# Kernel tuning notes

Measured on AMD Instinct MI355X. Metric: run time of the kernel, lower is better.

The kernel has to match this reference:

```python
import jax, jax.numpy as jnp
import numpy as np

N_USERS, N_MOVIES, M, K = 100000, 20000, 8, 32
B = 524288

def setup_inputs() -> dict:
    key = jax.random.key(0)
    k1, k2, k3, k4 = jax.random.split(key, 4)
    edge = jax.random.randint(k1, (B, 2), 0, 20000, dtype=jnp.int64) if jax.config.jax_enable_x64 else jax.random.randint(k1, (B, 2), 0, 20000, dtype=jnp.int32)
    std = 1.0 / K
    taste_emb = jax.random.normal(k2, (N_USERS, M * K), dtype=jnp.float32) * std
    attn_emb = jax.random.normal(k3, (N_USERS, M * K), dtype=jnp.float32) * std
    movie_emb = jax.random.normal(k4, (N_MOVIES, K), dtype=jnp.float32) * std
    user_bias = jnp.zeros((N_USERS, 1), dtype=jnp.float32)
    movie_bias = jnp.zeros((N_MOVIES, 1), dtype=jnp.float32)
    return {"edge": edge, "taste_emb": taste_emb, "attn_emb": attn_emb,
            "movie_emb": movie_emb, "user_bias": user_bias, "movie_bias": movie_bias}

def reference(edge, taste_emb, attn_emb, movie_emb, user_bias, movie_bias):
    u = edge[:, 0]
    v = edge[:, 1]
    A = attn_emb[u].reshape(-1, M, K)   # [B, m, k]
    U = taste_emb[u].reshape(-1, M, K)  # [B, m, k]
    e = movie_emb[v]                    # [B, k]
    logits = jnp.einsum('bmk,bk->bm', A, e)          # bmm(A, e) -> [B, m]
    att = jax.nn.softmax(logits, axis=1)             # softmax over m tastes
    scores = jnp.einsum('bmk,bk->bm', U, e)          # bmm(U, e) -> [B, m]
    y_hat = jnp.sum(scores * att, axis=1) + movie_bias[v, 0] + user_bias[u, 0]
    return y_hat  # [B]
```

## Files before the change

### kernel.cpp

```cpp
#include <hip/hip_runtime.h>


#define MOT_CAP     64
#define MOT_OVF_CAP 4096

__device__ __forceinline__ float mot_score(const float* __restrict__ Ar,
                                           const float* __restrict__ Tr,
                                           const float4* __restrict__ Ep) {
    float4 ek[8];
    #pragma unroll
    for (int k4 = 0; k4 < 8; ++k4) ek[k4] = Ep[k4];
    float num = 0.f, den = 0.f;
    #pragma unroll
    for (int m = 0; m < 8; ++m) {
        float l = 0.f, s = 0.f;
        #pragma unroll
        for (int k4 = 0; k4 < 8; ++k4) {
            const float4 a = *(const float4*)(Ar + m * 32 + k4 * 4);
            const float4 t = *(const float4*)(Tr + m * 32 + k4 * 4);
            const float4 e = ek[k4];
            l = fmaf(a.x, e.x, l); l = fmaf(a.y, e.y, l);
            l = fmaf(a.z, e.z, l); l = fmaf(a.w, e.w, l);
            s = fmaf(t.x, e.x, s); s = fmaf(t.y, e.y, s);
            s = fmaf(t.z, e.z, s); s = fmaf(t.w, e.w, s);
        }
        const float ex = __expf(l);
        den += ex;
        num = fmaf(ex, s, num);
    }
    return num / den;
}

__global__ void mot_scatter_kernel(const int4* __restrict__ edge2,
                                   int* __restrict__ cnt,
                                   int* __restrict__ ovfMeta,
                                   int* __restrict__ ovf,
                                   int2* __restrict__ sve,
                                   int nPairs, int nEdges) {
    const int i = blockIdx.x * 256 + (int)threadIdx.x;
    if (i < nPairs) {
        const int4 q = edge2[i];
        int pos = atomicAdd(&cnt[q.x], 1);
        if (pos < MOT_CAP) sve[(size_t)q.x * MOT_CAP + pos] = make_int2(q.y, 2 * i);
        else { int o = atomicAdd(ovfMeta, 1); if (o < MOT_OVF_CAP) ovf[o] = 2 * i; }
        pos = atomicAdd(&cnt[q.z], 1);
        if (pos < MOT_CAP) sve[(size_t)q.z * MOT_CAP + pos] = make_int2(q.w, 2 * i + 1);
        else { int o = atomicAdd(ovfMeta, 1); if (o < MOT_OVF_CAP) ovf[o] = 2 * i + 1; }
    } else if (i == nPairs && (nEdges & 1)) {
        const int2 e = ((const int2*)edge2)[nEdges - 1];
        int pos = atomicAdd(&cnt[e.x], 1);
        if (pos < MOT_CAP) sve[(size_t)e.x * MOT_CAP + pos] = make_int2(e.y, nEdges - 1);
        else { int o = atomicAdd(ovfMeta, 1); if (o < MOT_OVF_CAP) ovf[o] = nEdges - 1; }
    }
}

__global__ __launch_bounds__(256, 4) void mot_main_kernel(
    const int2* __restrict__ edge,
    const float* __restrict__ taste_emb,
    const float* __restrict__ attn_emb,
    const float4* __restrict__ movie_emb,
    const float* __restrict__ user_bias,
    const float* __restrict__ movie_bias,
    const int* __restrict__ cnt,
    const int2* __restrict__ sve,
    const int* __restrict__ ovfMeta,
    const int* __restrict__ ovf,
    float* __restrict__ out,
    int nUsers)
{
    const int lane = (int)threadIdx.x & 63;
    const int wid  = blockIdx.x * 4 + ((int)threadIdx.x >> 6);

    if (wid < nUsers) {
        const int u = __builtin_amdgcn_readfirstlane(wid);
        int n = cnt[u];
        n = n > MOT_CAP ? MOT_CAP : n;
        if (n == 0) return;
        int2 ve = make_int2(0, -1);
        if (lane < n) ve = sve[(size_t)u * MOT_CAP + lane];
        const float y = mot_score(attn_emb  + (size_t)u * 256,
                                  taste_emb + (size_t)u * 256,
                                  movie_emb + (size_t)ve.x * 8)
                        + user_bias[u] + movie_bias[ve.x];
        if (ve.y >= 0) out[ve.y] = y;
    } else {
        int oc = ovfMeta[0];
        if (oc > MOT_OVF_CAP) oc = MOT_OVF_CAP;
        const int oi = (wid - nUsers) * 64 + lane;
        if (oi < oc) {
            const int eid = ovf[oi];
            const int2 ed = edge[eid];
            out[eid] = mot_score(attn_emb  + (size_t)ed.x * 256,
                                 taste_emb + (size_t)ed.x * 256,
                                 movie_emb + (size_t)ed.y * 8)
                       + user_bias[ed.x] + movie_bias[ed.y];
        }
    }
}

__global__ __launch_bounds__(256, 4) void mot_flat_kernel(
    const int2* __restrict__ edge,
    const float4* __restrict__ taste_emb,
    const float4* __restrict__ attn_emb,
    const float4* __restrict__ movie_emb,
    const float* __restrict__ user_bias,
    const float* __restrict__ movie_bias,
    float* __restrict__ out,
    int nEdges)
{
    const int tid  = blockIdx.x * 256 + (int)threadIdx.x;
    const int eid  = tid >> 5;
    const int s    = tid & 31;
    if (eid >= nEdges) return;
    const int2 ed = edge[eid];
    const int u = ed.x, v = ed.y;
    const float4* Ap = attn_emb  + (size_t)u * 64;
    const float4* Tp = taste_emb + (size_t)u * 64;
    const float4* Ep = movie_emb + (size_t)v * 8;
    const float4 a0 = Ap[2 * s], a1 = Ap[2 * s + 1];
    const float4 t0 = Tp[2 * s], t1 = Tp[2 * s + 1];
    const int c = s & 3;
    const float4 e0 = Ep[2 * c], e1 = Ep[2 * c + 1];
    float lp = a0.x*e0.x + a0.y*e0.y + a0.z*e0.z + a0.w*e0.w
             + a1.x*e1.x + a1.y*e1.y + a1.z*e1.z + a1.w*e1.w;
    float sp = t0.x*e0.x + t0.y*e0.y + t0.z*e0.z + t0.w*e0.w
             + t1.x*e1.x + t1.y*e1.y + t1.z*e1.z + t1.w*e1.w;
    lp += __shfl_xor(lp, 1); lp += __shfl_xor(lp, 2);
    sp += __shfl_xor(sp, 1); sp += __shfl_xor(sp, 2);
    const float ex = __expf(lp);
    float den = ex, num = ex * sp;
    den += __shfl_xor(den, 4);  num += __shfl_xor(num, 4);
    den += __shfl_xor(den, 8);  num += __shfl_xor(num, 8);
    den += __shfl_xor(den, 16); num += __shfl_xor(num, 16);
    if (s == 0) out[eid] = num / den + user_bias[u] + movie_bias[v];
}

extern "C" void kernel_launch(void* const* d_in, const int* in_sizes, int n_in,
                              void* d_out, int out_size, void* d_ws, size_t ws_size,
                              hipStream_t stream) {
    const int2*   edge       = (const int2*)d_in[0];
    const float*  taste_emb  = (const float*)d_in[1];
    const float*  attn_emb   = (const float*)d_in[2];
    const float*  movie_emb  = (const float*)d_in[3];
    const float*  user_bias  = (const float*)d_in[4];
    const float*  movie_bias = (const float*)d_in[5];
    float*        out        = (float*)d_out;

    const int nEdges = in_sizes[0] / 2;
    const int NB     = in_sizes[3] / 32;

    auto align256 = [](size_t x) { return (x + 255) & ~(size_t)255; };
    char* ws = (char*)d_ws;

    const size_t o_cnt  = 0;
    const size_t o_meta = align256((size_t)NB * 4);
    const size_t o_ovf  = o_meta + 256;
    const size_t o_sve  = align256(o_ovf + (size_t)MOT_OVF_CAP * 4);
    const size_t need   = o_sve + (size_t)NB * MOT_CAP * 8;

    if (ws_size < need) {
        const int blocks = (nEdges * 32 + 255) / 256;
        mot_flat_kernel<<<blocks, 256, 0, stream>>>(
            edge, (const float4*)taste_emb, (const float4*)attn_emb,
            (const float4*)movie_emb, user_bias, movie_bias, out, nEdges);
        return;
    }

    int*  cnt     = (int*)(ws + o_cnt);
    int*  ovfMeta = (int*)(ws + o_meta);
    int*  ovf     = (int*)(ws + o_ovf);
    int2* sve     = (int2*)(ws + o_sve);

    hipMemsetAsync(ws, 0, o_ovf, stream);

    const int nPairs  = nEdges / 2;
    const int sblocks = (nPairs + 1 + 255) / 256;
    mot_scatter_kernel<<<sblocks, 256, 0, stream>>>(
        (const int4*)edge, cnt, ovfMeta, ovf, sve, nPairs, nEdges);

    const int ublocks = (NB + 3) / 4 + (MOT_OVF_CAP / 64 + 3) / 4;
    mot_main_kernel<<<ublocks, 256, 0, stream>>>(
        edge, taste_emb, attn_emb, (const float4*)movie_emb,
        user_bias, movie_bias, cnt, sve, ovfMeta, ovf, out, NB);
}
```

Measured before the change: 72.17 us.

## Stage user embedding rows in LDS and process half-wave per user

Each block now loads the attn and taste rows of 8 users cooperatively into shared memory, and each half-wave (32 lanes) handles one user's bucket, looping over edges in chunks of 32. The per-edge inner loop reads the user rows from LDS instead of through wave-uniform global loads, and the division is replaced by a hardware reciprocal. The change targets the scalar/global load overhead of reading 2 KB per user per lane group, and gives better lane use for users with at most 32 edges. In exchange it adds a barrier, 16 KB of LDS per block, and possible LDS bank conflicts from broadcast float4 reads.

```diff
diff --git a/kernel.cpp b/kernel.cpp
--- a/kernel.cpp
+++ b/kernel.cpp
@@ -4,9 +4,9 @@
 #define MOT_CAP     64
 #define MOT_OVF_CAP 4096
 
-__device__ __forceinline__ float mot_score(const float* __restrict__ Ar,
-                                           const float* __restrict__ Tr,
-                                           const float4* __restrict__ Ep) {
+__device__ __forceinline__ float mot_score_div(const float* __restrict__ Ar,
+                                               const float* __restrict__ Tr,
+                                               const float4* __restrict__ Ep) {
     float4 ek[8];
     #pragma unroll
     for (int k4 = 0; k4 < 8; ++k4) ek[k4] = Ep[k4];
@@ -66,33 +66,79 @@
     const int* __restrict__ ovfMeta,
     const int* __restrict__ ovf,
     float* __restrict__ out,
-    int nUsers)
+    int nUsers, int mainBlocks)
 {
-    const int lane = (int)threadIdx.x & 63;
-    const int wid  = blockIdx.x * 4 + ((int)threadIdx.x >> 6);
-
-    if (wid < nUsers) {
-        const int u = __builtin_amdgcn_readfirstlane(wid);
+    __shared__ float4 sA[8 * 64];
+    __shared__ float4 sT[8 * 64];
+
+    const int tid = (int)threadIdx.x;
+
+    if ((int)blockIdx.x < mainBlocks) {
+        const int u0 = (int)blockIdx.x * 8;
+        const int nu = (nUsers - u0) < 8 ? (nUsers - u0) : 8;
+        {
+            const float4* __restrict__ srcA = (const float4*)(attn_emb)  + (size_t)u0 * 64;
+            const float4* __restrict__ srcT = (const float4*)(taste_emb) + (size_t)u0 * 64;
+            const int nf = nu * 64;
+            for (int i = tid; i < nf; i += 256) { sA[i] = srcA[i]; sT[i] = srcT[i]; }
+        }
+        __syncthreads();
+
+        const int lane = tid & 63;
+        const int us   = (tid >> 6) * 2 + (lane >> 5);
+        const int s    = lane & 31;
+        const int u    = u0 + us;
+        if (us >= nu) return;
+
         int n = cnt[u];
         n = n > MOT_CAP ? MOT_CAP : n;
         if (n == 0) return;
-        int2 ve = make_int2(0, -1);
-        if (lane < n) ve = sve[(size_t)u * MOT_CAP + lane];
-        const float y = mot_score(attn_emb  + (size_t)u * 256,
-                                  taste_emb + (size_t)u * 256,
-                                  movie_emb + (size_t)ve.x * 8)
-                        + user_bias[u] + movie_bias[ve.x];
-        if (ve.y >= 0) out[ve.y] = y;
+
+        const float  ub = user_bias[u];
+        const float4* __restrict__ Arow = sA + us * 64;
+        const float4* __restrict__ Trow = sT + us * 64;
+        const int2*  __restrict__ bucket = sve + (size_t)u * MOT_CAP;
+
+        for (int base = 0; base < n; base += 32) {
+            const int ei = base + s;
+            if (ei < n) {
+                const int2 ve = bucket[ei];
+                const float4* __restrict__ Ep = movie_emb + (size_t)ve.x * 8;
+                float4 ek[8];
+                #pragma unroll
+                for (int k4 = 0; k4 < 8; ++k4) ek[k4] = Ep[k4];
+
+                float num = 0.f, den = 0.f;
+                #pragma unroll
+                for (int m = 0; m < 8; ++m) {
+                    float l = 0.f, sc = 0.f;
+                    #pragma unroll
+                    for (int k4 = 0; k4 < 8; ++k4) {
+                        const float4 a = Arow[m * 8 + k4];
+                        const float4 t = Trow[m * 8 + k4];
+                        const float4 e = ek[k4];
+                        l  = fmaf(a.x, e.x, l);  l  = fmaf(a.y, e.y, l);
+                        l  = fmaf(a.z, e.z, l);  l  = fmaf(a.w, e.w, l);
+                        sc = fmaf(t.x, e.x, sc); sc = fmaf(t.y, e.y, sc);
+                        sc = fmaf(t.z, e.z, sc); sc = fmaf(t.w, e.w, sc);
+                    }
+                    const float ex = __expf(l);
+                    den += ex;
+                    num = fmaf(ex, sc, num);
+                }
+                out[ve.y] = num * __builtin_amdgcn_rcpf(den) + ub + movie_bias[ve.x];
+            }
+        }
     } else {
         int oc = ovfMeta[0];
         if (oc > MOT_OVF_CAP) oc = MOT_OVF_CAP;
-        const int oi = (wid - nUsers) * 64 + lane;
+        const int oi = ((int)blockIdx.x - mainBlocks) * 256 + tid;
         if (oi < oc) {
             const int eid = ovf[oi];
             const int2 ed = edge[eid];
-            out[eid] = mot_score(attn_emb  + (size_t)ed.x * 256,
-                                 taste_emb + (size_t)ed.x * 256,
-                                 movie_emb + (size_t)ed.y * 8)
+            out[eid] = mot_score_div(attn_emb  + (size_t)ed.x * 256,
+                                     taste_emb + (size_t)ed.x * 256,
+                                     movie_emb + (size_t)ed.y * 8)
                        + user_bias[ed.x] + movie_bias[ed.y];
         }
     }
@@ -178,8 +224,9 @@
     mot_scatter_kernel<<<sblocks, 256, 0, stream>>>(
         (const int4*)edge, cnt, ovfMeta, ovf, sve, nPairs, nEdges);
 
-    const int ublocks = (NB + 3) / 4 + (MOT_OVF_CAP / 64 + 3) / 4;
-    mot_main_kernel<<<ublocks, 256, 0, stream>>>(
+    const int mainBlocks = (NB + 7) / 8;
+    const int ovfBlocks  = MOT_OVF_CAP / 256;
+    mot_main_kernel<<<mainBlocks + ovfBlocks, 256, 0, stream>>>(
         edge, taste_emb, attn_emb, (const float4*)movie_emb,
-        user_bias, movie_bias, cnt, sve, ovfMeta, ovf, out, NB);
-}
+        user_bias, movie_bias, cnt, sve, ovfMeta, ovf, out, NB, mainBlocks);
+}
```

Measured after the change: 72.68 us. Within noise of the previous version (+0.7%).

## Replace capped per-user buckets with counting sort of edges by user

Applied to the files above, without the earlier changes.

Swaps the fixed-capacity per-user bucket scatter plus overflow list for an exact counting sort. The new pipeline is histogram, single-block scan, then scatter into a dense sorted array. A flat per-edge kernel then processes edges in user order, so neighbouring threads share user rows in cache. This removes the idle lanes that came from one wavefront per user with few edges, and drops the overflow path. In exchange it adds two extra kernel launches and a serial single-block scan over 20000 entries.

```diff
diff --git a/kernel.cpp b/kernel.cpp
--- a/kernel.cpp
+++ b/kernel.cpp
@@ -1,101 +1,109 @@
 #include <hip/hip_runtime.h>
 
 
-#define MOT_CAP     64
-#define MOT_OVF_CAP 4096
+__global__ void mot_zero_kernel(int4* __restrict__ p, int n4) {
+    const int i = blockIdx.x * 256 + (int)threadIdx.x;
+    if (i < n4) p[i] = make_int4(0, 0, 0, 0);
+}
 
-__device__ __forceinline__ float mot_score(const float* __restrict__ Ar,
-                                           const float* __restrict__ Tr,
-                                           const float4* __restrict__ Ep) {
+__global__ void mot_hist_kernel(const int4* __restrict__ edge2, int* __restrict__ hist,
+                                int nPairs, int nEdges) {
+    const int i = blockIdx.x * 256 + (int)threadIdx.x;
+    if (i < nPairs) {
+        const int4 q = edge2[i];
+        atomicAdd(&hist[q.x], 1);
+        atomicAdd(&hist[q.z], 1);
+    } else if (i == nPairs && (nEdges & 1)) {
+        atomicAdd(&hist[((const int2*)edge2)[nEdges - 1].x], 1);
+    }
+}
+
+__global__ __launch_bounds__(1024) void mot_scan_kernel(const int* __restrict__ hist,
+                                                        int* __restrict__ cursor, int n) {
+    const int T = 1024;
+    const int t = (int)threadIdx.x;
+    const int chunk = (n + T - 1) / T;
+    const int lo = t * chunk;
+    const int hi = (lo + chunk) < n ? (lo + chunk) : n;
+    int sum = 0;
+    for (int i = lo; i < hi; ++i) sum += hist[i];
+
+    const int lane = t & 63, w = t >> 6;
+    int incl = sum;
+    for (int off = 1; off < 64; off <<= 1) {
+        int x = __shfl_up(incl, off);
+        if (lane >= off) incl += x;
+    }
+    __shared__ int wsum[16];
+    if (lane == 63) wsum[w] = incl;
+    __syncthreads();
+    int woff = 0;
+    for (int k = 0; k < w; ++k) woff += wsum[k];
+    int run = woff + incl - sum;
+    for (int i = lo; i < hi; ++i) {
+        cursor[i] = run;
+        run += hist[i];
+    }
+}
+
+__global__ void mot_scatter_kernel(const int4* __restrict__ edge2, int* __restrict__ cursor,
+                                   int4* __restrict__ sve4, int nPairs, int nEdges) {
+    const int i = blockIdx.x * 256 + (int)threadIdx.x;
+    if (i < nPairs) {
+        const int4 q = edge2[i];
+        int pos = atomicAdd(&cursor[q.x], 1);
+        sve4[pos] = make_int4(q.x, q.y, 2 * i, 0);
+        pos = atomicAdd(&cursor[q.z], 1);
+        sve4[pos] = make_int4(q.z, q.w, 2 * i + 1, 0);
+    } else if (i == nPairs && (nEdges & 1)) {
+        const int2 e = ((const int2*)edge2)[nEdges - 1];
+        int pos = atomicAdd(&cursor[e.x], 1);
+        sve4[pos] = make_int4(e.x, e.y, nEdges - 1, 0);
+    }
+}
+
+__global__ __launch_bounds__(256, 4) void mot_edge_kernel(
+    const int4* __restrict__ sve4,
+    const float4* __restrict__ taste_emb,
+    const float4* __restrict__ attn_emb,
+    const float4* __restrict__ movie_emb,
+    const float* __restrict__ user_bias,
+    const float* __restrict__ movie_bias,
+    float* __restrict__ out,
+    int nEdges)
+{
+    const int i = blockIdx.x * 256 + (int)threadIdx.x;
+    if (i >= nEdges) return;
+    const int4 e = sve4[i];
+
+    const float4* __restrict__ Ap = attn_emb  + (size_t)e.x * 64;
+    const float4* __restrict__ Tp = taste_emb + (size_t)e.x * 64;
+    const float4* __restrict__ Ep = movie_emb + (size_t)e.y * 8;
+
     float4 ek[8];
     #pragma unroll
     for (int k4 = 0; k4 < 8; ++k4) ek[k4] = Ep[k4];
+
     float num = 0.f, den = 0.f;
     #pragma unroll
     for (int m = 0; m < 8; ++m) {
+        float4 av[8], tv[8];
+        #pragma unroll
+        for (int k4 = 0; k4 < 8; ++k4) { av[k4] = Ap[m * 8 + k4]; tv[k4] = Tp[m * 8 + k4]; }
         float l = 0.f, s = 0.f;
         #pragma unroll
         for (int k4 = 0; k4 < 8; ++k4) {
-            const float4 a = *(const float4*)(Ar + m * 32 + k4 * 4);
-            const float4 t = *(const float4*)(Tr + m * 32 + k4 * 4);
-            const float4 e = ek[k4];
-            l = fmaf(a.x, e.x, l); l = fmaf(a.y, e.y, l);
-            l = fmaf(a.z, e.z, l); l = fmaf(a.w, e.w, l);
-            s = fmaf(t.x, e.x, s); s = fmaf(t.y, e.y, s);
-            s = fmaf(t.z, e.z, s); s = fmaf(t.w, e.w, s);
+            const float4 a = av[k4], t = tv[k4], v = ek[k4];
+            l = fmaf(a.x, v.x, l); l = fmaf(a.y, v.y, l);
+            l = fmaf(a.z, v.z, l); l = fmaf(a.w, v.w, l);
+            s = fmaf(t.x, v.x, s); s = fmaf(t.y, v.y, s);
+            s = fmaf(t.z, v.z, s); s = fmaf(t.w, v.w, s);
         }
         const float ex = __expf(l);
         den += ex;
         num = fmaf(ex, s, num);
     }
-    return num / den;
-}
-
-__global__ void mot_scatter_kernel(const int4* __restrict__ edge2,
-                                   int* __restrict__ cnt,
-                                   int* __restrict__ ovfMeta,
-                                   int* __restrict__ ovf,
-                                   int2* __restrict__ sve,
-                                   int nPairs, int nEdges) {
-    const int i = blockIdx.x * 256 + (int)threadIdx.x;
-    if (i < nPairs) {
-        const int4 q = edge2[i];
-        int pos = atomicAdd(&cnt[q.x], 1);
-        if (pos < MOT_CAP) sve[(size_t)q.x * MOT_CAP + pos] = make_int2(q.y, 2 * i);
-        else { int o = atomicAdd(ovfMeta, 1); if (o < MOT_OVF_CAP) ovf[o] = 2 * i; }
-        pos = atomicAdd(&cnt[q.z], 1);
-        if (pos < MOT_CAP) sve[(size_t)q.z * MOT_CAP + pos] = make_int2(q.w, 2 * i + 1);
-        else { int o = atomicAdd(ovfMeta, 1); if (o < MOT_OVF_CAP) ovf[o] = 2 * i + 1; }
-    } else if (i == nPairs && (nEdges & 1)) {
-        const int2 e = ((const int2*)edge2)[nEdges - 1];
-        int pos = atomicAdd(&cnt[e.x], 1);
-        if (pos < MOT_CAP) sve[(size_t)e.x * MOT_CAP + pos] = make_int2(e.y, nEdges - 1);
-        else { int o = atomicAdd(ovfMeta, 1); if (o < MOT_OVF_CAP) ovf[o] = nEdges - 1; }
-    }
-}
-
-__global__ __launch_bounds__(256, 4) void mot_main_kernel(
-    const int2* __restrict__ edge,
-    const float* __restrict__ taste_emb,
-    const float* __restrict__ attn_emb,
-    const float4* __restrict__ movie_emb,
-    const float* __restrict__ user_bias,
-    const float* __restrict__ movie_bias,
-    const int* __restrict__ cnt,
-    const int2* __restrict__ sve,
-    const int* __restrict__ ovfMeta,
-    const int* __restrict__ ovf,
-    float* __restrict__ out,
-    int nUsers)
-{
-    const int lane = (int)threadIdx.x & 63;
-    const int wid  = blockIdx.x * 4 + ((int)threadIdx.x >> 6);
-
-    if (wid < nUsers) {
-        const int u = __builtin_amdgcn_readfirstlane(wid);
-        int n = cnt[u];
-        n = n > MOT_CAP ? MOT_CAP : n;
-        if (n == 0) return;
-        int2 ve = make_int2(0, -1);
-        if (lane < n) ve = sve[(size_t)u * MOT_CAP + lane];
-        const float y = mot_score(attn_emb  + (size_t)u * 256,
-                                  taste_emb + (size_t)u * 256,
-                                  movie_emb + (size_t)ve.x * 8)
-                        + user_bias[u] + movie_bias[ve.x];
-        if (ve.y >= 0) out[ve.y] = y;
-    } else {
-        int oc = ovfMeta[0];
-        if (oc > MOT_OVF_CAP) oc = MOT_OVF_CAP;
-        const int oi = (wid - nUsers) * 64 + lane;
-        if (oi < oc) {
-            const int eid = ovf[oi];
-            const int2 ed = edge[eid];
-            out[eid] = mot_score(attn_emb  + (size_t)ed.x * 256,
-                                 taste_emb + (size_t)ed.x * 256,
-                                 movie_emb + (size_t)ed.y * 8)
-                       + user_bias[ed.x] + movie_bias[ed.y];
-        }
-    }
+    out[e.z] = num * __builtin_amdgcn_rcpf(den) + user_bias[e.x] + movie_bias[e.y];
 }
 
 __global__ __launch_bounds__(256, 4) void mot_flat_kernel(
@@ -152,11 +160,10 @@
     auto align256 = [](size_t x) { return (x + 255) & ~(size_t)255; };
     char* ws = (char*)d_ws;
 
-    const size_t o_cnt  = 0;
-    const size_t o_meta = align256((size_t)NB * 4);
-    const size_t o_ovf  = o_meta + 256;
-    const size_t o_sve  = align256(o_ovf + (size_t)MOT_OVF_CAP * 4);
-    const size_t need   = o_sve + (size_t)NB * MOT_CAP * 8;
+    const size_t o_hist = 0;
+    const size_t o_cur  = align256((size_t)NB * 4);
+    const size_t o_sve  = align256(o_cur + (size_t)NB * 4);
+    const size_t need   = o_sve + (size_t)nEdges * 16;
 
     if (ws_size < need) {
         const int blocks = (nEdges * 32 + 255) / 256;
@@ -166,20 +173,22 @@
         return;
     }
 
-    int*  cnt     = (int*)(ws + o_cnt);
-    int*  ovfMeta = (int*)(ws + o_meta);
-    int*  ovf     = (int*)(ws + o_ovf);
-    int2* sve     = (int2*)(ws + o_sve);
+    int*  hist   = (int*)(ws + o_hist);
+    int*  cursor = (int*)(ws + o_cur);
+    int4* sve4   = (int4*)(ws + o_sve);
 
-    hipMemsetAsync(ws, 0, o_ovf, stream);
+    const int n4 = (int)(align256((size_t)NB * 4) / 16);
+    mot_zero_kernel<<<(n4 + 255) / 256, 256, 0, stream>>>((int4*)hist, n4);
 
     const int nPairs  = nEdges / 2;
     const int sblocks = (nPairs + 1 + 255) / 256;
-    mot_scatter_kernel<<<sblocks, 256, 0, stream>>>(
-        (const int4*)edge, cnt, ovfMeta, ovf, sve, nPairs, nEdges);
+    mot_hist_kernel<<<sblocks, 256, 0, stream>>>((const int4*)edge, hist, nPairs, nEdges);
+    mot_scan_kernel<<<1, 1024, 0, stream>>>(hist, cursor, NB);
+    mot_scatter_kernel<<<sblocks, 256, 0, stream>>>((const int4*)edge, cursor, sve4,
+                                                    nPairs, nEdges);
 
-    const int ublocks = (NB + 3) / 4 + (MOT_OVF_CAP / 64 + 3) / 4;
-    mot_main_kernel<<<ublocks, 256, 0, stream>>>(
-        edge, taste_emb, attn_emb, (const float4*)movie_emb,
-        user_bias, movie_bias, cnt, sve, ovfMeta, ovf, out, NB);
+    const int eblocks = (nEdges + 255) / 256;
+    mot_edge_kernel<<<eblocks, 256, 0, stream>>>(
+        sve4, (const float4*)taste_emb, (const float4*)attn_emb,
+        (const float4*)movie_emb, user_bias, movie_bias, out, nEdges);
 }
```

New measurement: 141.3 us. 95.7% more time.

## Compute per-user logits with fp16 MFMA and replace memset with zero kernel

Applied to the files above, without the earlier changes.

The per-user main kernel now loads each user's 16 attention and taste rows once into an fp16 MFMA A-operand. It processes up to 16 movies per 16x16x32 MFMA, then redistributes the results with lane shuffles for the softmax. This replaces the per-lane scalar FMA loops, where every lane re-read the full 2 KB of user rows. It also swaps hipMemsetAsync for a custom zero kernel and uses a reciprocal instead of division. The fp16 conversion of embeddings and the approximate reciprocal reduce numerical precision.

```diff
diff --git a/kernel.cpp b/kernel.cpp
--- a/kernel.cpp
+++ b/kernel.cpp
@@ -4,9 +4,17 @@
 #define MOT_CAP     64
 #define MOT_OVF_CAP 4096
 
-__device__ __forceinline__ float mot_score(const float* __restrict__ Ar,
-                                           const float* __restrict__ Tr,
-                                           const float4* __restrict__ Ep) {
+using half8 = __attribute__((ext_vector_type(8))) _Float16;
+using f32x4 = __attribute__((ext_vector_type(4))) float;
+
+__global__ void mot_zero_kernel(int4* __restrict__ p, int n4) {
+    const int i = blockIdx.x * 256 + (int)threadIdx.x;
+    if (i < n4) p[i] = make_int4(0, 0, 0, 0);
+}
+
+__device__ __forceinline__ float mot_score_div(const float* __restrict__ Ar,
+                                               const float* __restrict__ Tr,
+                                               const float4* __restrict__ Ep) {
     float4 ek[8];
     #pragma unroll
     for (int k4 = 0; k4 < 8; ++k4) ek[k4] = Ep[k4];
@@ -54,7 +62,7 @@
     }
 }
 
-__global__ __launch_bounds__(256, 4) void mot_main_kernel(
+__global__ __launch_bounds__(256, 4) void mot_mfma_kernel(
     const int2* __restrict__ edge,
     const float* __restrict__ taste_emb,
     const float* __restrict__ attn_emb,
@@ -66,33 +74,92 @@
     const int* __restrict__ ovfMeta,
     const int* __restrict__ ovf,
     float* __restrict__ out,
-    int nUsers)
+    int nUsers, int mainBlocks)
 {
-    const int lane = (int)threadIdx.x & 63;
-    const int wid  = blockIdx.x * 4 + ((int)threadIdx.x >> 6);
-
-    if (wid < nUsers) {
-        const int u = __builtin_amdgcn_readfirstlane(wid);
+    const int tid  = (int)threadIdx.x;
+    const int lane = tid & 63;
+
+    if ((int)blockIdx.x < mainBlocks) {
+        const int u = (int)blockIdx.x * 4 + (tid >> 6);
+        if (u >= nUsers) return;
         int n = cnt[u];
         n = n > MOT_CAP ? MOT_CAP : n;
         if (n == 0) return;
-        int2 ve = make_int2(0, -1);
-        if (lane < n) ve = sve[(size_t)u * MOT_CAP + lane];
-        const float y = mot_score(attn_emb  + (size_t)u * 256,
-                                  taste_emb + (size_t)u * 256,
-                                  movie_emb + (size_t)ve.x * 8)
-                        + user_bias[u] + movie_bias[ve.x];
-        if (ve.y >= 0) out[ve.y] = y;
+
+        const int row = lane & 15;
+        const int kq  = lane >> 4;
+        const int k0  = kq * 8;
+
+        const float* rowp = (row < 8)
+            ? attn_emb  + (size_t)u * 256 + row * 32 + k0
+            : taste_emb + (size_t)u * 256 + (row - 8) * 32 + k0;
+        const float4 r0 = *(const float4*)rowp;
+        const float4 r1 = *(const float4*)(rowp + 4);
+        half8 af;
+        af[0] = (_Float16)r0.x; af[1] = (_Float16)r0.y;
+        af[2] = (_Float16)r0.z; af[3] = (_Float16)r0.w;
+        af[4] = (_Float16)r1.x; af[5] = (_Float16)r1.y;
+        af[6] = (_Float16)r1.z; af[7] = (_Float16)r1.w;
+
+        const float ub = user_bias[u];
+        const int2* __restrict__ bucket = sve + (size_t)u * MOT_CAP;
+        const int hi = kq & 1;
+
+        for (int t = 0; t < n; t += 16) {
+            const int ei = t + row;
+            const bool valid = ei < n;
+            const int2 ve = valid ? bucket[ei] : make_int2(0, -1);
+
+            half8 bf = {};
+            if (valid) {
+                const float4* __restrict__ Ep = movie_emb + (size_t)ve.x * 8;
+                const float4 e0 = Ep[kq * 2];
+                const float4 e1 = Ep[kq * 2 + 1];
+                bf[0] = (_Float16)e0.x; bf[1] = (_Float16)e0.y;
+                bf[2] = (_Float16)e0.z; bf[3] = (_Float16)e0.w;
+                bf[4] = (_Float16)e1.x; bf[5] = (_Float16)e1.y;
+                bf[6] = (_Float16)e1.z; bf[7] = (_Float16)e1.w;
+            }
+
+            f32x4 c = {0.f, 0.f, 0.f, 0.f};
+            c = __builtin_amdgcn_mfma_f32_16x16x32_f16(af, bf, c, 0, 0, 0);
+
+            const float o0 = __shfl_xor(c[0], 16);
+            const float o1 = __shfl_xor(c[1], 16);
+            const float o2 = __shfl_xor(c[2], 16);
+            const float o3 = __shfl_xor(c[3], 16);
+            float v0 = hi ? o0 : c[0], v1 = hi ? o1 : c[1];
+            float v2 = hi ? o2 : c[2], v3 = hi ? o3 : c[3];
+            float v4 = hi ? c[0] : o0, v5 = hi ? c[1] : o1;
+            float v6 = hi ? c[2] : o2, v7 = hi ? c[3] : o3;
+            const float w0 = __shfl_xor(v0, 32), w1 = __shfl_xor(v1, 32);
+            const float w2 = __shfl_xor(v2, 32), w3 = __shfl_xor(v3, 32);
+            const float w4 = __shfl_xor(v4, 32), w5 = __shfl_xor(v5, 32);
+            const float w6 = __shfl_xor(v6, 32), w7 = __shfl_xor(v7, 32);
+
+            if (kq == 0 && valid) {
+                float den = 0.f, num = 0.f;
+                const float e0x = __expf(v0); den += e0x; num = fmaf(e0x, w0, num);
+                const float e1x = __expf(v1); den += e1x; num = fmaf(e1x, w1, num);
+                const float e2x = __expf(v2); den += e2x; num = fmaf(e2x, w2, num);
+                const float e3x = __expf(v3); den += e3x; num = fmaf(e3x, w3, num);
+                const float e4x = __expf(v4); den += e4x; num = fmaf(e4x, w4, num);
+                const float e5x = __expf(v5); den += e5x; num = fmaf(e5x, w5, num);
+                const float e6x = __expf(v6); den += e6x; num = fmaf(e6x, w6, num);
+                const float e7x = __expf(v7); den += e7x; num = fmaf(e7x, w7, num);
+                out[ve.y] = num * __builtin_amdgcn_rcpf(den) + ub + movie_bias[ve.x];
+            }
+        }
     } else {
         int oc = ovfMeta[0];
         if (oc > MOT_OVF_CAP) oc = MOT_OVF_CAP;
-        const int oi = (wid - nUsers) * 64 + lane;
+        const int oi = ((int)blockIdx.x - mainBlocks) * 256 + tid;
         if (oi < oc) {
             const int eid = ovf[oi];
             const int2 ed = edge[eid];
-            out[eid] = mot_score(attn_emb  + (size_t)ed.x * 256,
-                                 taste_emb + (size_t)ed.x * 256,
-                                 movie_emb + (size_t)ed.y * 8)
+            out[eid] = mot_score_div(attn_emb  + (size_t)ed.x * 256,
+                                     taste_emb + (size_t)ed.x * 256,
+                                     movie_emb + (size_t)ed.y * 8)
                        + user_bias[ed.x] + movie_bias[ed.y];
         }
     }
@@ -171,15 +238,17 @@
     int*  ovf     = (int*)(ws + o_ovf);
     int2* sve     = (int2*)(ws + o_sve);
 
-    hipMemsetAsync(ws, 0, o_ovf, stream);
+    const int n4 = (int)(o_ovf / 16);
+    mot_zero_kernel<<<(n4 + 255) / 256, 256, 0, stream>>>((int4*)ws, n4);
 
     const int nPairs  = nEdges / 2;
     const int sblocks = (nPairs + 1 + 255) / 256;
     mot_scatter_kernel<<<sblocks, 256, 0, stream>>>(
         (const int4*)edge, cnt, ovfMeta, ovf, sve, nPairs, nEdges);
 
-    const int ublocks = (NB + 3) / 4 + (MOT_OVF_CAP / 64 + 3) / 4;
-    mot_main_kernel<<<ublocks, 256, 0, stream>>>(
+    const int mainBlocks = (NB + 3) / 4;
+    const int ovfBlocks  = MOT_OVF_CAP / 256;
+    mot_mfma_kernel<<<mainBlocks + ovfBlocks, 256, 0, stream>>>(
         edge, taste_emb, attn_emb, (const float4*)movie_emb,
-        user_bias, movie_bias, cnt, sve, ovfMeta, ovf, out, NB);
-}
+        user_bias, movie_bias, cnt, sve, ovfMeta, ovf, out, NB, mainBlocks);
+}
```

Measured after the change: 65.48 us. -9.3%, faster.
